# Performance work log

Hardware: AMD Instinct MI355X
Metric: run time of the kernel (lower is better)

The kernel has to match this reference:

```python
import jax, jax.numpy as jnp
import numpy as np

N_NODES = 50000
N_EDGES = 800000
IN_C, HID_C, OUT_C = 256, 256, 128


def gcn_conv(x, W, b, row, col, n_nodes):
    """PyG GCNConv: linear transform, symmetric-normalized aggregation, bias.
    row/col already include self-loops. Messages flow row -> col."""
    h = x @ W  # [N, out]
    deg = jax.ops.segment_sum(jnp.ones_like(col, dtype=h.dtype), col, num_segments=n_nodes)
    d_inv_sqrt = jnp.where(deg > 0, jax.lax.rsqrt(jnp.maximum(deg, 1e-12)), 0.0)
    norm = d_inv_sqrt[row] * d_inv_sqrt[col]  # [E]
    msg = h[row] * norm[:, None]              # gather + scale, [E, out]
    out = jax.ops.segment_sum(msg, col, num_segments=n_nodes)  # scatter-add
    return out + b


def setup_inputs() -> dict:
    key = jax.random.key(0)
    k_x, k_e, k_w1, k_w2 = jax.random.split(key, 4)
    x = jax.random.normal(k_x, (N_NODES, IN_C), dtype=jnp.float32)
    edge_index = jax.random.randint(k_e, (2, N_EDGES), 0, N_NODES, dtype=jnp.int64)
    # Glorot-style init for GCN weights, zeros bias (PyG default)
    s1 = float(np.sqrt(6.0 / (IN_C + HID_C)))
    s2 = float(np.sqrt(6.0 / (HID_C + OUT_C)))
    W1 = jax.random.uniform(k_w1, (IN_C, HID_C), dtype=jnp.float32, minval=-s1, maxval=s1)
    b1 = jnp.zeros((HID_C,), dtype=jnp.float32)
    W2 = jax.random.uniform(k_w2, (HID_C, OUT_C), dtype=jnp.float32, minval=-s2, maxval=s2)
    b2 = jnp.zeros((OUT_C,), dtype=jnp.float32)
    return {"x": x, "edge_index": edge_index, "W1": W1, "b1": b1, "W2": W2, "b2": b2}


def reference(x, edge_index, W1, b1, W2, b2):
    n = x.shape[0]
    # add self-loops (PyG GCNConv default add_self_loops=True)
    loops = jnp.arange(n, dtype=edge_index.dtype)
    row = jnp.concatenate([edge_index[0], loops])
    col = jnp.concatenate([edge_index[1], loops])
    h = gcn_conv(x, W1, b1, row, col, n)
    h = jax.nn.relu(h)  # dropout p=0.0 -> identity
    out = gcn_conv(h, W2, b2, row, col, n)
    return out
```

## Files before the change

### kernel.cpp

```cpp
#include <hip/hip_runtime.h>

#define NN 50000
#define NE 800000
#define IN_C 256
#define HID_C 256
#define OUT_C 128

#define NBUCK 196
#define CHUNK 4096
#define NPA 196
#define CAP_B 5120

typedef unsigned short u16;
typedef __attribute__((ext_vector_type(8))) short short8;
typedef __attribute__((ext_vector_type(8))) unsigned short ushort8;
typedef __attribute__((ext_vector_type(4))) float f32x4;

__device__ __forceinline__ u16 f2b(float f) {
  unsigned int u = __float_as_uint(f);
  return (u16)((u + 0x7FFFu + ((u >> 16) & 1u)) >> 16);
}
__device__ __forceinline__ float b2f(u16 s) {
  return __uint_as_float(((unsigned int)s) << 16);
}


__global__ __launch_bounds__(256) void convw_zero(const float* __restrict__ W1,
                                                  const float* __restrict__ W2,
                                                  u16* __restrict__ W1t,
                                                  u16* __restrict__ W2t,
                                                  int* __restrict__ cnt) {
  int b = blockIdx.x;
  if (b < 256) {
    int id = b * 256 + threadIdx.x;
    if (id < 256 * 256) {
      int n = id >> 8, k = id & 255;
      W1t[id] = f2b(W1[k * 256 + n]);
    }
    if (id < 128 * 256) {
      int n = id >> 8, k = id & 255;
      W2t[id] = f2b(W2[k * 128 + n]);
    }
  } else {
    int i = (b - 256) * 256 + threadIdx.x;
    if (i < NN) cnt[i] = 0;
  }
}


__global__ __launch_bounds__(256) void hist_kernel(const int* __restrict__ col,
                                                   int* __restrict__ cnt, int E) {
  int e = blockIdx.x * blockDim.x + threadIdx.x;
  if (e < E) atomicAdd(&cnt[col[e]], 1);
}

__global__ __launch_bounds__(256) void scan1_kernel(const int* __restrict__ cnt,
                                                    int* __restrict__ bsum, int n) {
  __shared__ int ws[4];
  int i = blockIdx.x * 256 + threadIdx.x;
  int lane = threadIdx.x & 63, wid = threadIdx.x >> 6;
  int v = (i < n) ? cnt[i] : 0;
#pragma unroll
  for (int off = 32; off > 0; off >>= 1) v += __shfl_down(v, off, 64);
  if (lane == 0) ws[wid] = v;
  __syncthreads();
  if (threadIdx.x == 0) bsum[blockIdx.x] = ws[0] + ws[1] + ws[2] + ws[3];
}

__global__ __launch_bounds__(256) void scan2_kernel(const int* __restrict__ bsum,
                                                    int* __restrict__ boff,
                                                    int* __restrict__ row_off,
                                                    int nb, int n) {
  __shared__ int wsum[4], wpre[5];
  int lane = threadIdx.x & 63, wid = threadIdx.x >> 6;
  int v = (threadIdx.x < nb) ? bsum[threadIdx.x] : 0;
  int s = v;
#pragma unroll
  for (int off = 1; off < 64; off <<= 1) {
    int t = __shfl_up(s, off, 64);
    if (lane >= off) s += t;
  }
  if (lane == 63) wsum[wid] = s;
  __syncthreads();
  if (threadIdx.x == 0) {
    int acc = 0;
#pragma unroll
    for (int w = 0; w < 4; ++w) { wpre[w] = acc; acc += wsum[w]; }
    wpre[4] = acc;
  }
  __syncthreads();
  if (threadIdx.x < nb) boff[threadIdx.x] = wpre[wid] + (s - v);
  if (threadIdx.x == 0) row_off[n] = wpre[4];
}

__global__ __launch_bounds__(256) void scan3_kernel(const int* __restrict__ cnt,
                                                    const int* __restrict__ boff,
                                                    int* __restrict__ row_off,
                                                    int* __restrict__ bcur,
                                                    float* __restrict__ dinv, int n) {
  __shared__ int wsum[4], wpre[4];
  int i = blockIdx.x * 256 + threadIdx.x;
  int lane = threadIdx.x & 63, wid = threadIdx.x >> 6;
  int v = (i < n) ? cnt[i] : 0;
  int s = v;
#pragma unroll
  for (int off = 1; off < 64; off <<= 1) {
    int t = __shfl_up(s, off, 64);
    if (lane >= off) s += t;
  }
  if (lane == 63) wsum[wid] = s;
  __syncthreads();
  if (threadIdx.x == 0) {
    int acc = 0;
#pragma unroll
    for (int w = 0; w < 4; ++w) { wpre[w] = acc; acc += wsum[w]; }
  }
  __syncthreads();
  if (i < n) {
    int off = boff[blockIdx.x] + wpre[wid] + (s - v);
    row_off[i] = off;
    if ((i & 255) == 0) bcur[i >> 8] = off;
    dinv[i] = rsqrtf((float)(v + 1));
  }
}


template <bool A_IS_F32>
__device__ __forceinline__ void gemm_body(const void* __restrict__ Ap,
                                          const u16* __restrict__ Bt,
                                          const float* __restrict__ dscale,
                                          u16* __restrict__ C, int M, int N,
                                          int bx, int by,
                                          u16 (&Asl)[2][5120], u16 (&Bsl)[2][5120]) {
  const int tid = threadIdx.x;
  const int row0 = by * 128;
  const int col0 = bx * 128;

  f32x4 acc[4][4] = {};

  const int seg = tid & 7;
  const int rb = tid >> 3;
  const int wave = tid >> 6, lane = tid & 63;
  const int wm = wave >> 1, wn = wave & 1;
  const int qr = lane & 15, quad = lane >> 4;

  float4 aF[4];
  ushort4 aU[4];
  ushort4 bR[4];

  auto load_tiles = [&](int k0) {
    if constexpr (A_IS_F32) {
      const float* A = (const float*)Ap;
#pragma unroll
      for (int i = 0; i < 4; ++i) {
        int gr = row0 + rb + i * 32;
        aF[i] = (gr < M) ? *(const float4*)&A[(size_t)gr * 256 + k0 + seg * 4]
                         : make_float4(0.f, 0.f, 0.f, 0.f);
      }
    } else {
      const u16* A = (const u16*)Ap;
#pragma unroll
      for (int i = 0; i < 4; ++i) {
        int gr = row0 + rb + i * 32;
        aU[i] = (gr < M) ? *(const ushort4*)&A[(size_t)gr * 256 + k0 + seg * 4]
                         : make_ushort4(0, 0, 0, 0);
      }
    }
#pragma unroll
    for (int i = 0; i < 4; ++i) {
      int n = rb + i * 32;
      bR[i] = *(const ushort4*)&Bt[(size_t)(col0 + n) * 256 + k0 + seg * 4];
    }
  };

  auto write_lds = [&](int buf) {
#pragma unroll
    for (int i = 0; i < 4; ++i) {
      int r = rb + i * 32;
      ushort4 u;
      if constexpr (A_IS_F32) {
        u.x = f2b(aF[i].x); u.y = f2b(aF[i].y);
        u.z = f2b(aF[i].z); u.w = f2b(aF[i].w);
      } else {
        u = aU[i];
      }
      *(ushort4*)&Asl[buf][r * 40 + seg * 4] = u;
      *(ushort4*)&Bsl[buf][r * 40 + seg * 4] = bR[i];
    }
  };

  load_tiles(0);
  write_lds(0);
  __syncthreads();

#pragma unroll
  for (int it = 0; it < 8; ++it) {
    const int cur = it & 1;
    if (it < 7) load_tiles((it + 1) * 32);

    short8 afr[4], bfr[4];
#pragma unroll
    for (int mt = 0; mt < 4; ++mt)
      afr[mt] = *(const short8*)&Asl[cur][(wm * 64 + mt * 16 + qr) * 40 + quad * 8];
#pragma unroll
    for (int nt = 0; nt < 4; ++nt)
      bfr[nt] = *(const short8*)&Bsl[cur][(wn * 64 + nt * 16 + qr) * 40 + quad * 8];
#pragma unroll
    for (int mt = 0; mt < 4; ++mt)
#pragma unroll
      for (int nt = 0; nt < 4; ++nt)
        acc[mt][nt] = __builtin_amdgcn_mfma_f32_16x16x32_bf16(afr[mt], bfr[nt], acc[mt][nt], 0, 0, 0);

    if (it < 7) {
      write_lds(1 - cur);
      __syncthreads();
    }
  }

#pragma unroll
  for (int mt = 0; mt < 4; ++mt) {
#pragma unroll
    for (int i = 0; i < 4; ++i) {
      int gr = row0 + wm * 64 + mt * 16 + quad * 4 + i;
      if (gr < M) {
        float sc = dscale[gr];
#pragma unroll
        for (int nt = 0; nt < 4; ++nt) {
          int gc = col0 + wn * 64 + nt * 16 + qr;
          C[(size_t)gr * N + gc] = f2b(acc[mt][nt][i] * sc);
        }
      }
    }
  }
}

template <bool A_IS_F32>
__global__ __launch_bounds__(256) void gemm_mfma(const void* __restrict__ Ap,
                                                 const u16* __restrict__ Bt,
                                                 const float* __restrict__ dscale,
                                                 u16* __restrict__ C, int M, int N) {
  __shared__ u16 Asl[2][5120];
  __shared__ u16 Bsl[2][5120];
  gemm_body<A_IS_F32>(Ap, Bt, dscale, C, M, N, blockIdx.x, blockIdx.y, Asl, Bsl);
}

__global__ __launch_bounds__(256) void gemm1_scatter(const float* __restrict__ x,
                                                     const u16* __restrict__ W1t,
                                                     const float* __restrict__ dinv,
                                                     u16* __restrict__ Hb, int M, int N,
                                                     int ngb,
                                                     const int* __restrict__ row,
                                                     const int* __restrict__ col,
                                                     int* __restrict__ bcur,
                                                     uint2* __restrict__ stage, int E) {
  __shared__ u16 ABsl[4][5120];
  int b = blockIdx.x;
  if (b < ngb) {
    gemm_body<true>(x, W1t, dinv, Hb, M, N, b & 1, b >> 1,
                    *reinterpret_cast<u16(*)[2][5120]>(&ABsl[0]),
                    *reinterpret_cast<u16(*)[2][5120]>(&ABsl[2]));
  } else {
    uint2* pairs = (uint2*)ABsl;
    int* hcnt = (int*)((char*)ABsl + 32768);
    int* hscan = hcnt + 256;
    int* hbase = hscan + 256;
    int* lcur = hbase + 256;

    const int tid = threadIdx.x;
    const int blk = b - ngb;
    const int e0 = blk * CHUNK;

    hcnt[tid] = 0;
    __syncthreads();

    int ecol[16], erow[16];
#pragma unroll
    for (int j = 0; j < 16; ++j) {
      int e = e0 + j * 256 + tid;
      if (e < E) {
        ecol[j] = col[e];
        erow[j] = row[e];
        atomicAdd(&hcnt[ecol[j] >> 8], 1);
      } else {
        ecol[j] = -1;
      }
    }
    __syncthreads();

    hscan[tid] = hcnt[tid];
    __syncthreads();
#pragma unroll
    for (int off = 1; off < 256; off <<= 1) {
      int t = (tid >= off) ? hscan[tid - off] : 0;
      __syncthreads();
      hscan[tid] += t;
      __syncthreads();
    }

    lcur[tid] = 0;
    if (hcnt[tid] > 0) hbase[tid] = atomicAdd(&bcur[tid], hcnt[tid]);
    __syncthreads();

#pragma unroll
    for (int j = 0; j < 16; ++j) {
      if (ecol[j] >= 0) {
        int bk = ecol[j] >> 8;
        int p = atomicAdd(&lcur[bk], 1);
        pairs[(hscan[bk] - hcnt[bk]) + p] = make_uint2((unsigned)erow[j], (unsigned)ecol[j]);
      }
    }
    __syncthreads();

    int mtot = hscan[255];
    for (int s = tid; s < mtot; s += 256) {
      uint2 pr = pairs[s];
      int bk = (int)(pr.y >> 8);
      stage[hbase[bk] + (s - (hscan[bk] - hcnt[bk]))] = pr;
    }
  }
}

__global__ __launch_bounds__(256) void csr_sort(const uint2* __restrict__ stage,
                                                const int* __restrict__ row_off,
                                                int* __restrict__ csr) {
  __shared__ int cur[256];
  __shared__ int outb[CAP_B];
  const int b = blockIdx.x;
  const int base_node = b << 8;
  const int nnodes = min(256, NN - base_node);
  const int tid = threadIdx.x;
  const int bstart = row_off[base_node];
  const int bend = row_off[min(base_node + 256, NN)];
  if (tid < nnodes) cur[tid] = row_off[base_node + tid] - bstart;
  __syncthreads();
  const int m = bend - bstart;
  for (int i = tid; i < m; i += 256) {
    uint2 pr = stage[bstart + i];
    int cl = (int)pr.y - base_node;
    int p = atomicAdd(&cur[cl], 1);
    if (p < CAP_B) outb[p] = (int)pr.x;
    else csr[bstart + p] = (int)pr.x;
  }
  __syncthreads();
  const int mm = min(m, CAP_B);
  for (int i = tid; i < mm; i += 256) csr[bstart + i] = outb[i];
}


__global__ __launch_bounds__(256) void agg256_bf(const u16* __restrict__ h,
                                                 const int* __restrict__ row_off,
                                                 const int* __restrict__ csr,
                                                 const float* __restrict__ dinv,
                                                 const float* __restrict__ bias,
                                                 u16* __restrict__ out, int n) {
  int wave = threadIdx.x >> 6;
  int lane = threadIdx.x & 63;
  int half = lane >> 5;
  int sl = lane & 31;
  int v = blockIdx.x * 8 + wave * 2 + half;
  if (v >= n) return;
  int beg = row_off[v], end = row_off[v + 1];
  float a[8] = {};
  int e = beg;
  for (; e < end && (e & 3); ++e) {
    int s0 = csr[e];
    ushort8 g0 = *(const ushort8*)&h[(size_t)s0 * 256 + sl * 8];
#pragma unroll
    for (int i = 0; i < 8; ++i) a[i] += b2f((u16)g0[i]);
  }
  for (; e + 7 < end; e += 8) {
    int4 i0 = *(const int4*)&csr[e];
    int4 i1 = *(const int4*)&csr[e + 4];
    int s[8] = {i0.x, i0.y, i0.z, i0.w, i1.x, i1.y, i1.z, i1.w};
    ushort8 g[8];
#pragma unroll
    for (int j = 0; j < 8; ++j)
      g[j] = *(const ushort8*)&h[(size_t)s[j] * 256 + sl * 8];
#pragma unroll
    for (int j = 0; j < 8; ++j)
#pragma unroll
      for (int i = 0; i < 8; ++i) a[i] += b2f((u16)g[j][i]);
  }
  for (; e < end; ++e) {
    int s0 = csr[e];
    ushort8 g0 = *(const ushort8*)&h[(size_t)s0 * 256 + sl * 8];
#pragma unroll
    for (int i = 0; i < 8; ++i) a[i] += b2f((u16)g0[i]);
  }
  ushort8 hs = *(const ushort8*)&h[(size_t)v * 256 + sl * 8];
#pragma unroll
  for (int i = 0; i < 8; ++i) a[i] += b2f((u16)hs[i]);
  float dv = dinv[v];
  float4 bv0 = *(const float4*)&bias[sl * 8];
  float4 bv1 = *(const float4*)&bias[sl * 8 + 4];
  float bb[8] = {bv0.x, bv0.y, bv0.z, bv0.w, bv1.x, bv1.y, bv1.z, bv1.w};
  ushort8 o;
#pragma unroll
  for (int i = 0; i < 8; ++i) {
    float r = fmaxf(a[i] * dv + bb[i], 0.f);
    o[i] = (short)f2b(r);
  }
  *(ushort8*)&out[(size_t)v * 256 + sl * 8] = o;
}

__global__ __launch_bounds__(256) void agg128_bf(const u16* __restrict__ h,
                                                 const int* __restrict__ row_off,
                                                 const int* __restrict__ csr,
                                                 const float* __restrict__ dinv,
                                                 const float* __restrict__ bias,
                                                 float* __restrict__ out, int n) {
  int wave = threadIdx.x >> 6;
  int lane = threadIdx.x & 63;
  int quarter = lane >> 4;
  int sl = lane & 15;
  int v = blockIdx.x * 16 + wave * 4 + quarter;
  if (v >= n) return;
  int beg = row_off[v], end = row_off[v + 1];
  float a[8] = {};
  int e = beg;
  for (; e < end && (e & 3); ++e) {
    int s0 = csr[e];
    ushort8 g0 = *(const ushort8*)&h[(size_t)s0 * 128 + sl * 8];
#pragma unroll
    for (int i = 0; i < 8; ++i) a[i] += b2f((u16)g0[i]);
  }
  for (; e + 7 < end; e += 8) {
    int4 i0 = *(const int4*)&csr[e];
    int4 i1 = *(const int4*)&csr[e + 4];
    int s[8] = {i0.x, i0.y, i0.z, i0.w, i1.x, i1.y, i1.z, i1.w};
    ushort8 g[8];
#pragma unroll
    for (int j = 0; j < 8; ++j)
      g[j] = *(const ushort8*)&h[(size_t)s[j] * 128 + sl * 8];
#pragma unroll
    for (int j = 0; j < 8; ++j)
#pragma unroll
      for (int i = 0; i < 8; ++i) a[i] += b2f((u16)g[j][i]);
  }
  for (; e < end; ++e) {
    int s0 = csr[e];
    ushort8 g0 = *(const ushort8*)&h[(size_t)s0 * 128 + sl * 8];
#pragma unroll
    for (int i = 0; i < 8; ++i) a[i] += b2f((u16)g0[i]);
  }
  ushort8 hs = *(const ushort8*)&h[(size_t)v * 128 + sl * 8];
#pragma unroll
  for (int i = 0; i < 8; ++i) a[i] += b2f((u16)hs[i]);
  float dv = dinv[v];
  float4 bv0 = *(const float4*)&bias[sl * 8];
  float4 bv1 = *(const float4*)&bias[sl * 8 + 4];
  float bb[8] = {bv0.x, bv0.y, bv0.z, bv0.w, bv1.x, bv1.y, bv1.z, bv1.w};
  float o[8];
#pragma unroll
  for (int i = 0; i < 8; ++i) o[i] = a[i] * dv + bb[i];
  *(float4*)&out[(size_t)v * 128 + sl * 8] = make_float4(o[0], o[1], o[2], o[3]);
  *(float4*)&out[(size_t)v * 128 + sl * 8 + 4] = make_float4(o[4], o[5], o[6], o[7]);
}


extern "C" void kernel_launch(void* const* d_in, const int* in_sizes, int n_in,
                              void* d_out, int out_size, void* d_ws, size_t ws_size,
                              hipStream_t stream) {
  const float* x = (const float*)d_in[0];
  const int* ei = (const int*)d_in[1];
  const float* W1 = (const float*)d_in[2];
  const float* b1 = (const float*)d_in[3];
  const float* W2 = (const float*)d_in[4];
  const float* b2 = (const float*)d_in[5];
  float* out = (float*)d_out;

  const int* row = ei;
  const int* col = ei + NE;

  const int NB = (NN + 255) / 256;

  u16* Hb = (u16*)d_ws;
  u16* H2b = Hb + (size_t)NN * 256;
  u16* H3b = H2b + (size_t)NN * 256;
  u16* W1t = H3b + (size_t)NN * 128;
  u16* W2t = W1t + 256 * 256;
  int* cnt = (int*)(W2t + 128 * 256);
  int* row_off = cnt + NN;
  int* bcur = row_off + NN + 4;
  float* dinv = (float*)(bcur + 256);
  int* bsum = (int*)(dinv + NN);
  int* boff = bsum + 200;
  int* csr = boff + 200;
  uint2* stage = (uint2*)H3b;

  convw_zero<<<256 + NB, 256, 0, stream>>>(W1, W2, W1t, W2t, cnt);
  hist_kernel<<<(NE + 255) / 256, 256, 0, stream>>>(col, cnt, NE);
  scan1_kernel<<<NB, 256, 0, stream>>>(cnt, bsum, NN);
  scan2_kernel<<<1, 256, 0, stream>>>(bsum, boff, row_off, NB, NN);
  scan3_kernel<<<NB, 256, 0, stream>>>(cnt, boff, row_off, bcur, dinv, NN);

  {
    const int ngb = (HID_C / 128) * ((NN + 127) / 128);
    gemm1_scatter<<<ngb + NPA, 256, 0, stream>>>(x, W1t, dinv, Hb, NN, HID_C, ngb,
                                                 row, col, bcur, stage, NE);
  }
  csr_sort<<<NBUCK, 256, 0, stream>>>(stage, row_off, csr);
  agg256_bf<<<(NN + 7) / 8, 256, 0, stream>>>(Hb, row_off, csr, dinv, b1, H2b, NN);

  {
    dim3 grid(OUT_C / 128, (NN + 127) / 128);
    gemm_mfma<false><<<grid, 256, 0, stream>>>(H2b, W2t, dinv, H3b, NN, OUT_C);
  }
  agg128_bf<<<(NN + 15) / 16, 256, 0, stream>>>(H3b, row_off, csr, dinv, b2, out, NN);
}
```

Measured before the change: 293.4 us.

## Assign one wavefront per node in aggregation with shuffled neighbor indices and zero pad row

Both aggregation kernels now give a whole wavefront to each destination node instead of half or a quarter of a wave. The wave loads 16 neighbor indices at once, broadcasts them with shuffles, and lets sub-groups of lanes gather different neighbors in parallel, then combines the partial sums with xor-shuffles. Out-of-range slots point to an extra zeroed padding row at index NN, which the init kernel now clears, so the tail loops are gone. This raises gather parallelism per node and memory-level concurrency, at the cost of more waves, idle lanes for low-degree nodes, and shuffle reductions.

```diff
diff --git a/kernel.cpp b/kernel.cpp
--- a/kernel.cpp
+++ b/kernel.cpp
@@ -29,7 +29,10 @@
                                                   const float* __restrict__ W2,
                                                   u16* __restrict__ W1t,
                                                   u16* __restrict__ W2t,
-                                                  int* __restrict__ cnt) {
+                                                  int* __restrict__ cnt,
+                                                  u16* __restrict__ Hbz,
+                                                  u16* __restrict__ H3z,
+                                                  int nzb) {
   int b = blockIdx.x;
   if (b < 256) {
     int id = b * 256 + threadIdx.x;
@@ -41,9 +44,12 @@
       int n = id >> 8, k = id & 255;
       W2t[id] = f2b(W2[k * 128 + n]);
     }
-  } else {
+  } else if (b < 256 + nzb) {
     int i = (b - 256) * 256 + threadIdx.x;
     if (i < NN) cnt[i] = 0;
+  } else {
+    if (threadIdx.x < 256) Hbz[threadIdx.x] = 0;
+    if (threadIdx.x < 128) H3z[threadIdx.x] = 0;
   }
 }
 
@@ -357,50 +363,42 @@
   int lane = threadIdx.x & 63;
   int half = lane >> 5;
   int sl = lane & 31;
-  int v = blockIdx.x * 8 + wave * 2 + half;
+  int v = blockIdx.x * 4 + wave;
   if (v >= n) return;
   int beg = row_off[v], end = row_off[v + 1];
-  float a[8] = {};
-  int e = beg;
-  for (; e < end && (e & 3); ++e) {
-    int s0 = csr[e];
-    ushort8 g0 = *(const ushort8*)&h[(size_t)s0 * 256 + sl * 8];
-#pragma unroll
-    for (int i = 0; i < 8; ++i) a[i] += b2f((u16)g0[i]);
-  }
-  for (; e + 7 < end; e += 8) {
-    int4 i0 = *(const int4*)&csr[e];
-    int4 i1 = *(const int4*)&csr[e + 4];
-    int s[8] = {i0.x, i0.y, i0.z, i0.w, i1.x, i1.y, i1.z, i1.w};
+  ushort8 hs = *(const ushort8*)&h[(size_t)v * 256 + sl * 8];
+  float a[8];
+#pragma unroll
+  for (int i = 0; i < 8; ++i) a[i] = half ? 0.f : b2f((u16)hs[i]);
+  for (int e = beg; e < end; e += 16) {
+    int p = e + (lane & 15);
+    int idx = (p < end) ? csr[p] : NN;
     ushort8 g[8];
 #pragma unroll
+    for (int j = 0; j < 8; ++j) {
+      int s = __shfl(idx, 2 * j + half, 64);
+      g[j] = *(const ushort8*)&h[(size_t)s * 256 + sl * 8];
+    }
+#pragma unroll
     for (int j = 0; j < 8; ++j)
-      g[j] = *(const ushort8*)&h[(size_t)s[j] * 256 + sl * 8];
-#pragma unroll
-    for (int j = 0; j < 8; ++j)
 #pragma unroll
       for (int i = 0; i < 8; ++i) a[i] += b2f((u16)g[j][i]);
   }
-  for (; e < end; ++e) {
-    int s0 = csr[e];
-    ushort8 g0 = *(const ushort8*)&h[(size_t)s0 * 256 + sl * 8];
-#pragma unroll
-    for (int i = 0; i < 8; ++i) a[i] += b2f((u16)g0[i]);
-  }
-  ushort8 hs = *(const ushort8*)&h[(size_t)v * 256 + sl * 8];
-#pragma unroll
-  for (int i = 0; i < 8; ++i) a[i] += b2f((u16)hs[i]);
-  float dv = dinv[v];
-  float4 bv0 = *(const float4*)&bias[sl * 8];
-  float4 bv1 = *(const float4*)&bias[sl * 8 + 4];
-  float bb[8] = {bv0.x, bv0.y, bv0.z, bv0.w, bv1.x, bv1.y, bv1.z, bv1.w};
-  ushort8 o;
-#pragma unroll
-  for (int i = 0; i < 8; ++i) {
-    float r = fmaxf(a[i] * dv + bb[i], 0.f);
-    o[i] = (short)f2b(r);
-  }
-  *(ushort8*)&out[(size_t)v * 256 + sl * 8] = o;
+#pragma unroll
+  for (int i = 0; i < 8; ++i) a[i] += __shfl_xor(a[i], 32, 64);
+  if (half == 0) {
+    float dv = dinv[v];
+    float4 bv0 = *(const float4*)&bias[sl * 8];
+    float4 bv1 = *(const float4*)&bias[sl * 8 + 4];
+    float bb[8] = {bv0.x, bv0.y, bv0.z, bv0.w, bv1.x, bv1.y, bv1.z, bv1.w};
+    ushort8 o;
+#pragma unroll
+    for (int i = 0; i < 8; ++i) {
+      float r = fmaxf(a[i] * dv + bb[i], 0.f);
+      o[i] = (short)f2b(r);
+    }
+    *(ushort8*)&out[(size_t)v * 256 + sl * 8] = o;
+  }
 }
 
 __global__ __launch_bounds__(256) void agg128_bf(const u16* __restrict__ h,
@@ -413,48 +411,43 @@
   int lane = threadIdx.x & 63;
   int quarter = lane >> 4;
   int sl = lane & 15;
-  int v = blockIdx.x * 16 + wave * 4 + quarter;
+  int v = blockIdx.x * 4 + wave;
   if (v >= n) return;
   int beg = row_off[v], end = row_off[v + 1];
-  float a[8] = {};
-  int e = beg;
-  for (; e < end && (e & 3); ++e) {
-    int s0 = csr[e];
-    ushort8 g0 = *(const ushort8*)&h[(size_t)s0 * 128 + sl * 8];
-#pragma unroll
-    for (int i = 0; i < 8; ++i) a[i] += b2f((u16)g0[i]);
-  }
-  for (; e + 7 < end; e += 8) {
-    int4 i0 = *(const int4*)&csr[e];
-    int4 i1 = *(const int4*)&csr[e + 4];
-    int s[8] = {i0.x, i0.y, i0.z, i0.w, i1.x, i1.y, i1.z, i1.w};
-    ushort8 g[8];
-#pragma unroll
-    for (int j = 0; j < 8; ++j)
-      g[j] = *(const ushort8*)&h[(size_t)s[j] * 128 + sl * 8];
-#pragma unroll
-    for (int j = 0; j < 8; ++j)
+  ushort8 hs = *(const ushort8*)&h[(size_t)v * 128 + sl * 8];
+  float a[8];
+#pragma unroll
+  for (int i = 0; i < 8; ++i) a[i] = quarter ? 0.f : b2f((u16)hs[i]);
+  for (int e = beg; e < end; e += 16) {
+    int p = e + (lane & 15);
+    int idx = (p < end) ? csr[p] : NN;
+    ushort8 g[4];
+#pragma unroll
+    for (int j = 0; j < 4; ++j) {
+      int s = __shfl(idx, 4 * j + quarter, 64);
+      g[j] = *(const ushort8*)&h[(size_t)s * 128 + sl * 8];
+    }
+#pragma unroll
+    for (int j = 0; j < 4; ++j)
 #pragma unroll
       for (int i = 0; i < 8; ++i) a[i] += b2f((u16)g[j][i]);
   }
-  for (; e < end; ++e) {
-    int s0 = csr[e];
-    ushort8 g0 = *(const ushort8*)&h[(size_t)s0 * 128 + sl * 8];
-#pragma unroll
-    for (int i = 0; i < 8; ++i) a[i] += b2f((u16)g0[i]);
-  }
-  ushort8 hs = *(const ushort8*)&h[(size_t)v * 128 + sl * 8];
-#pragma unroll
-  for (int i = 0; i < 8; ++i) a[i] += b2f((u16)hs[i]);
-  float dv = dinv[v];
-  float4 bv0 = *(const float4*)&bias[sl * 8];
-  float4 bv1 = *(const float4*)&bias[sl * 8 + 4];
-  float bb[8] = {bv0.x, bv0.y, bv0.z, bv0.w, bv1.x, bv1.y, bv1.z, bv1.w};
-  float o[8];
-#pragma unroll
-  for (int i = 0; i < 8; ++i) o[i] = a[i] * dv + bb[i];
-  *(float4*)&out[(size_t)v * 128 + sl * 8] = make_float4(o[0], o[1], o[2], o[3]);
-  *(float4*)&out[(size_t)v * 128 + sl * 8 + 4] = make_float4(o[4], o[5], o[6], o[7]);
+#pragma unroll
+  for (int i = 0; i < 8; ++i) {
+    a[i] += __shfl_xor(a[i], 16, 64);
+    a[i] += __shfl_xor(a[i], 32, 64);
+  }
+  if (quarter == 0 && (lane >> 5) == 0) {
+    float dv = dinv[v];
+    float4 bv0 = *(const float4*)&bias[sl * 8];
+    float4 bv1 = *(const float4*)&bias[sl * 8 + 4];
+    float bb[8] = {bv0.x, bv0.y, bv0.z, bv0.w, bv1.x, bv1.y, bv1.z, bv1.w};
+    float o[8];
+#pragma unroll
+    for (int i = 0; i < 8; ++i) o[i] = a[i] * dv + bb[i];
+    *(float4*)&out[(size_t)v * 128 + sl * 8] = make_float4(o[0], o[1], o[2], o[3]);
+    *(float4*)&out[(size_t)v * 128 + sl * 8 + 4] = make_float4(o[4], o[5], o[6], o[7]);
+  }
 }
 
 
@@ -475,9 +468,9 @@
   const int NB = (NN + 255) / 256;
 
   u16* Hb = (u16*)d_ws;
-  u16* H2b = Hb + (size_t)NN * 256;
+  u16* H2b = Hb + (size_t)(NN + 1) * 256;
   u16* H3b = H2b + (size_t)NN * 256;
-  u16* W1t = H3b + (size_t)NN * 128;
+  u16* W1t = H3b + (size_t)(NN + 1) * 128;
   u16* W2t = W1t + 256 * 256;
   int* cnt = (int*)(W2t + 128 * 256);
   int* row_off = cnt + NN;
@@ -488,7 +481,9 @@
   int* csr = boff + 200;
   uint2* stage = (uint2*)H3b;
 
-  convw_zero<<<256 + NB, 256, 0, stream>>>(W1, W2, W1t, W2t, cnt);
+  convw_zero<<<256 + NB + 1, 256, 0, stream>>>(W1, W2, W1t, W2t, cnt,
+                                               Hb + (size_t)NN * 256,
+                                               H3b + (size_t)NN * 128, NB);
   hist_kernel<<<(NE + 255) / 256, 256, 0, stream>>>(col, cnt, NE);
   scan1_kernel<<<NB, 256, 0, stream>>>(cnt, bsum, NN);
   scan2_kernel<<<1, 256, 0, stream>>>(bsum, boff, row_off, NB, NN);
@@ -500,11 +495,11 @@
                                                  row, col, bcur, stage, NE);
   }
   csr_sort<<<NBUCK, 256, 0, stream>>>(stage, row_off, csr);
-  agg256_bf<<<(NN + 7) / 8, 256, 0, stream>>>(Hb, row_off, csr, dinv, b1, H2b, NN);
+  agg256_bf<<<(NN + 3) / 4, 256, 0, stream>>>(Hb, row_off, csr, dinv, b1, H2b, NN);
 
   {
     dim3 grid(OUT_C / 128, (NN + 127) / 128);
     gemm_mfma<false><<<grid, 256, 0, stream>>>(H2b, W2t, dinv, H3b, NN, OUT_C);
   }
-  agg128_bf<<<(NN + 15) / 16, 256, 0, stream>>>(H3b, row_off, csr, dinv, b2, out, NN);
-}
+  agg128_bf<<<(NN + 3) / 4, 256, 0, stream>>>(H3b, row_off, csr, dinv, b2, out, NN);
+}
```

After: 280.3 us. 4.5% less time.
